# Kernel optimization log

Hardware: AMD Instinct MI355X
Metric: run time of the kernel (lower is better)

## Reference

```python
import jax, jax.numpy as jnp
import numpy as np

N, M, D = 131072, 8, 128
TAU = 1.0
E_CONST = float(np.e)


def setup_inputs() -> dict:
    key = jax.random.key(0)
    ks = jax.random.split(key, 6)
    x = jax.random.normal(ks[0], (N, M, D), dtype=jnp.float32)
    q = jax.random.uniform(ks[1], (N, M), dtype=jnp.float32)  # per-mode energies
    w = 0.1 * jax.random.uniform(ks[2], (M,), dtype=jnp.float32)
    b = 0.1 * jax.random.uniform(ks[3], (M,), dtype=jnp.float32)
    gammas = jax.random.uniform(ks[4], (M, M), dtype=jnp.float32)  # in (0,1)
    G = 0.1 * jax.random.normal(ks[5], (M,), dtype=jnp.float32)
    bias = jnp.zeros((M,), dtype=jnp.float32)
    qmin = jnp.zeros((M,), dtype=jnp.float32)
    return {"x": x, "q": q, "w": w, "b": b, "gammas": gammas,
            "G": G, "bias": bias, "qmin": qmin}


def reference(x, q, w, b, gammas, G, bias, qmin):
    e = jnp.float32(E_CONST)
    # correction (eval mode): shift by running min, clamp at e so phi > 0
    corr = jnp.maximum(q - qmin[None, :] + e, e)          # [N, M]
    phi = (1.0 + w)[None, :] * corr + b[None, :]          # [N, M]
    # symmetrized gamma: g[i,j] = gammas[min(i,j), max(i,j)]
    idx = jnp.arange(gammas.shape[0])
    g_sym = jnp.where(idx[:, None] < idx[None, :], gammas, gammas.T)  # [M, M]
    # pairwise power-weighted partial energies: phi_i^g * phi_j^(1-g)
    partials = phi[:, :, None] ** g_sym[None] * phi[:, None, :] ** (1.0 - g_sym)[None]  # [N, M, M]
    modal = jnp.sum(partials, axis=-1)                    # [N, M]
    logs = jax.nn.log_softmax(-TAU * modal, axis=-1)
    alphas = jnp.exp(logs)                                # [N, M]
    # gated attention over modes
    betas = jax.nn.relu(jnp.tanh(G[None, :] * alphas + bias[None, :]))  # [N, M]
    return betas[:, :, None] * x                          # [N, M, D]
```

## Files before the change

kernel.cpp:

```cpp
#include <hip/hip_runtime.h>
#include <math.h>

#define NROWS 131072
#define M 8
#define D 128
#define ROWS_PER_BLOCK 128
#define E_CONST 2.71828182845904523536f

__global__ __launch_bounds__(256) void emma_fused_kernel(
    const float* __restrict__ x, const float* __restrict__ q,
    const float* __restrict__ w, const float* __restrict__ b,
    const float* __restrict__ gammas, const float* __restrict__ G,
    const float* __restrict__ bias, const float* __restrict__ qmin,
    float* __restrict__ out)
{
    __shared__ float s_beta[ROWS_PER_BLOCK][M];
    __shared__ float s_g[M][M];
    __shared__ float s_w[M], s_b[M], s_G[M], s_bias[M], s_qmin[M];

    const int tid = threadIdx.x;

    if (tid < M * M) {
        int i = tid >> 3, j = tid & 7;
        s_g[i][j] = (i < j) ? gammas[i * M + j] : gammas[j * M + i];
    }
    if (tid >= 64 && tid < 64 + M) {
        int m = tid - 64;
        s_w[m]    = w[m];
        s_b[m]    = b[m];
        s_G[m]    = G[m];
        s_bias[m] = bias[m];
        s_qmin[m] = qmin[m];
    }
    __syncthreads();

    const int row0 = blockIdx.x * ROWS_PER_BLOCK;

    if (tid < ROWS_PER_BLOCK) {
        const int n = row0 + tid;
        const float4 q0 = *reinterpret_cast<const float4*>(q + (size_t)n * M);
        const float4 q1 = *reinterpret_cast<const float4*>(q + (size_t)n * M + 4);
        float qv[M] = {q0.x, q0.y, q0.z, q0.w, q1.x, q1.y, q1.z, q1.w};

        float lphi[M];
        #pragma unroll
        for (int m = 0; m < M; ++m) {
            float corr = fmaxf(qv[m] - s_qmin[m] + E_CONST, E_CONST);
            float phi  = (1.0f + s_w[m]) * corr + s_b[m];
            lphi[m] = logf(phi);
        }

        float modal[M];
        #pragma unroll
        for (int i = 0; i < M; ++i) {
            float s = 0.0f;
            #pragma unroll
            for (int j = 0; j < M; ++j) {
                float g = s_g[i][j];
                s += expf(fmaf(g, lphi[i] - lphi[j], lphi[j]));
            }
            modal[i] = s;
        }

        float mx = -modal[0];
        #pragma unroll
        for (int i = 1; i < M; ++i) mx = fmaxf(mx, -modal[i]);
        float esum = 0.0f;
        float ea[M];
        #pragma unroll
        for (int i = 0; i < M; ++i) {
            ea[i] = expf(-modal[i] - mx);
            esum += ea[i];
        }
        float inv = 1.0f / esum;

        #pragma unroll
        for (int m = 0; m < M; ++m) {
            float alpha = ea[m] * inv;
            float t = tanhf(fmaf(s_G[m], alpha, s_bias[m]));
            s_beta[tid][m] = fmaxf(t, 0.0f);
        }
    }
    __syncthreads();

    const size_t base = (size_t)row0 * (M * D);
    const float4* __restrict__ x4 = reinterpret_cast<const float4*>(x + base);
    float4* __restrict__ o4       = reinterpret_cast<float4*>(out + base);
    const int mm = tid >> 5;

    #pragma unroll 4
    for (int r = 0; r < ROWS_PER_BLOCK; ++r) {
        const float beta = s_beta[r][mm];
        float4 v = x4[(size_t)r * 256 + tid];
        v.x *= beta; v.y *= beta; v.z *= beta; v.w *= beta;
        o4[(size_t)r * 256 + tid] = v;
    }
}

extern "C" void kernel_launch(void* const* d_in, const int* in_sizes, int n_in,
                              void* d_out, int out_size, void* d_ws, size_t ws_size,
                              hipStream_t stream) {
    const float* x      = (const float*)d_in[0];
    const float* q      = (const float*)d_in[1];
    const float* w      = (const float*)d_in[2];
    const float* b      = (const float*)d_in[3];
    const float* gammas = (const float*)d_in[4];
    const float* G      = (const float*)d_in[5];
    const float* bias   = (const float*)d_in[6];
    const float* qmin   = (const float*)d_in[7];
    float* out = (float*)d_out;

    const int grid = NROWS / ROWS_PER_BLOCK;
    emma_fused_kernel<<<grid, 256, 0, stream>>>(x, q, w, b, gammas, G, bias, qmin, out);
}
```

Measured before the change: 217.8 us.

## Split fused kernel into beta-computation and grid-stride scaling kernels

```diff
diff --git a/kernel.cpp b/kernel.cpp
--- a/kernel.cpp
+++ b/kernel.cpp
@@ -4,9 +4,88 @@
 #define NROWS 131072
 #define M 8
 #define D 128
-#define ROWS_PER_BLOCK 128
 #define E_CONST 2.71828182845904523536f
 
+__global__ __launch_bounds__(256) void emma_beta_kernel(
+    const float* __restrict__ q,
+    const float* __restrict__ w, const float* __restrict__ b,
+    const float* __restrict__ gammas, const float* __restrict__ G,
+    const float* __restrict__ bias, const float* __restrict__ qmin,
+    float* __restrict__ betas)
+{
+    const int n = blockIdx.x * 256 + threadIdx.x;
+    if (n >= NROWS) return;
+
+    const float4 q0 = *reinterpret_cast<const float4*>(q + (size_t)n * M);
+    const float4 q1 = *reinterpret_cast<const float4*>(q + (size_t)n * M + 4);
+    float qv[M] = {q0.x, q0.y, q0.z, q0.w, q1.x, q1.y, q1.z, q1.w};
+
+    float lphi[M];
+    #pragma unroll
+    for (int m = 0; m < M; ++m) {
+        float corr = fmaxf(qv[m] - qmin[m] + E_CONST, E_CONST);
+        float phi  = (1.0f + w[m]) * corr + b[m];
+        lphi[m] = logf(phi);
+    }
+
+    float modal[M];
+    #pragma unroll
+    for (int i = 0; i < M; ++i) {
+        float s = 0.0f;
+        #pragma unroll
+        for (int j = 0; j < M; ++j) {
+            float g = (i < j) ? gammas[i * M + j] : gammas[j * M + i];
+            s += expf(fmaf(g, lphi[i] - lphi[j], lphi[j]));
+        }
+        modal[i] = s;
+    }
+
+    float mx = -modal[0];
+    #pragma unroll
+    for (int i = 1; i < M; ++i) mx = fmaxf(mx, -modal[i]);
+    float esum = 0.0f;
+    float ea[M];
+    #pragma unroll
+    for (int i = 0; i < M; ++i) {
+        ea[i] = expf(-modal[i] - mx);
+        esum += ea[i];
+    }
+    float inv = 1.0f / esum;
+
+    float4 o0, o1;
+    float bo[M];
+    #pragma unroll
+    for (int m = 0; m < M; ++m) {
+        float alpha = ea[m] * inv;
+        float t = tanhf(fmaf(G[m], alpha, bias[m]));
+        bo[m] = fmaxf(t, 0.0f);
+    }
+    o0.x = bo[0]; o0.y = bo[1]; o0.z = bo[2]; o0.w = bo[3];
+    o1.x = bo[4]; o1.y = bo[5]; o1.z = bo[6]; o1.w = bo[7];
+    *reinterpret_cast<float4*>(betas + (size_t)n * M)     = o0;
+    *reinterpret_cast<float4*>(betas + (size_t)n * M + 4) = o1;
+}
+
+#define NV4 ((size_t)NROWS * M * D / 4)
+#define SB_BLOCKS 2048
+
+__global__ __launch_bounds__(256) void emma_scale_kernel(
+    const float4* __restrict__ x4,
+    const float* __restrict__ betas,
+    float4* __restrict__ o4)
+{
+    size_t i = (size_t)blockIdx.x * 256 + threadIdx.x;
+    const size_t stride = (size_t)SB_BLOCKS * 256;
+    #pragma unroll 4
+    for (int k = 0; k < (int)(NV4 / stride); ++k, i += stride) {
+        const float bta = betas[i >> 5];
+        float4 v = x4[i];
+        v.x *= bta; v.y *= bta; v.z *= bta; v.w *= bta;
+        o4[i] = v;
+    }
+}
+
+#define ROWS_PER_BLOCK 128
 __global__ __launch_bounds__(256) void emma_fused_kernel(
     const float* __restrict__ x, const float* __restrict__ q,
     const float* __restrict__ w, const float* __restrict__ b,
@@ -15,25 +94,7 @@
     float* __restrict__ out)
 {
     __shared__ float s_beta[ROWS_PER_BLOCK][M];
-    __shared__ float s_g[M][M];
-    __shared__ float s_w[M], s_b[M], s_G[M], s_bias[M], s_qmin[M];
-
     const int tid = threadIdx.x;
-
-    if (tid < M * M) {
-        int i = tid >> 3, j = tid & 7;
-        s_g[i][j] = (i < j) ? gammas[i * M + j] : gammas[j * M + i];
-    }
-    if (tid >= 64 && tid < 64 + M) {
-        int m = tid - 64;
-        s_w[m]    = w[m];
-        s_b[m]    = b[m];
-        s_G[m]    = G[m];
-        s_bias[m] = bias[m];
-        s_qmin[m] = qmin[m];
-    }
-    __syncthreads();
-
     const int row0 = blockIdx.x * ROWS_PER_BLOCK;
 
     if (tid < ROWS_PER_BLOCK) {
@@ -41,43 +102,35 @@
         const float4 q0 = *reinterpret_cast<const float4*>(q + (size_t)n * M);
         const float4 q1 = *reinterpret_cast<const float4*>(q + (size_t)n * M + 4);
         float qv[M] = {q0.x, q0.y, q0.z, q0.w, q1.x, q1.y, q1.z, q1.w};
-
         float lphi[M];
         #pragma unroll
         for (int m = 0; m < M; ++m) {
-            float corr = fmaxf(qv[m] - s_qmin[m] + E_CONST, E_CONST);
-            float phi  = (1.0f + s_w[m]) * corr + s_b[m];
+            float corr = fmaxf(qv[m] - qmin[m] + E_CONST, E_CONST);
+            float phi  = (1.0f + w[m]) * corr + b[m];
             lphi[m] = logf(phi);
         }
-
         float modal[M];
         #pragma unroll
         for (int i = 0; i < M; ++i) {
             float s = 0.0f;
             #pragma unroll
             for (int j = 0; j < M; ++j) {
-                float g = s_g[i][j];
+                float g = (i < j) ? gammas[i * M + j] : gammas[j * M + i];
                 s += expf(fmaf(g, lphi[i] - lphi[j], lphi[j]));
             }
             modal[i] = s;
         }
-
         float mx = -modal[0];
         #pragma unroll
         for (int i = 1; i < M; ++i) mx = fmaxf(mx, -modal[i]);
         float esum = 0.0f;
         float ea[M];
         #pragma unroll
-        for (int i = 0; i < M; ++i) {
-            ea[i] = expf(-modal[i] - mx);
-            esum += ea[i];
-        }
+        for (int i = 0; i < M; ++i) { ea[i] = expf(-modal[i] - mx); esum += ea[i]; }
         float inv = 1.0f / esum;
-
         #pragma unroll
         for (int m = 0; m < M; ++m) {
-            float alpha = ea[m] * inv;
-            float t = tanhf(fmaf(s_G[m], alpha, s_bias[m]));
+            float t = tanhf(fmaf(G[m], ea[m] * inv, bias[m]));
             s_beta[tid][m] = fmaxf(t, 0.0f);
         }
     }
@@ -87,7 +140,6 @@
     const float4* __restrict__ x4 = reinterpret_cast<const float4*>(x + base);
     float4* __restrict__ o4       = reinterpret_cast<float4*>(out + base);
     const int mm = tid >> 5;
-
     #pragma unroll 4
     for (int r = 0; r < ROWS_PER_BLOCK; ++r) {
         const float beta = s_beta[r][mm];
@@ -110,6 +162,15 @@
     const float* qmin   = (const float*)d_in[7];
     float* out = (float*)d_out;
 
-    const int grid = NROWS / ROWS_PER_BLOCK;
-    emma_fused_kernel<<<grid, 256, 0, stream>>>(x, q, w, b, gammas, G, bias, qmin, out);
+    const size_t beta_bytes = (size_t)NROWS * M * sizeof(float);
+    if (ws_size >= beta_bytes) {
+        float* betas = (float*)d_ws;
+        emma_beta_kernel<<<NROWS / 256, 256, 0, stream>>>(
+            q, w, b, gammas, G, bias, qmin, betas);
+        emma_scale_kernel<<<SB_BLOCKS, 256, 0, stream>>>(
+            (const float4*)x, betas, (float4*)out);
+    } else {
+        emma_fused_kernel<<<NROWS / ROWS_PER_BLOCK, 256, 0, stream>>>(
+            x, q, w, b, gammas, G, bias, qmin, out);
+    }
 }
```

After: 261.0 us. 19.8% more time.

## Spread modal softmax across 8 lanes per row with shuffle reductions

Applied to the files above, without the earlier changes.

```diff
diff --git a/kernel.cpp b/kernel.cpp
--- a/kernel.cpp
+++ b/kernel.cpp
@@ -4,40 +4,24 @@
 #define NROWS 131072
 #define M 8
 #define D 128
-#define ROWS_PER_BLOCK 128
+#define RPB 32
 #define E_CONST 2.71828182845904523536f
 
-__global__ __launch_bounds__(256) void emma_fused_kernel(
+__global__ __launch_bounds__(256) void emma_fused2(
     const float* __restrict__ x, const float* __restrict__ q,
     const float* __restrict__ w, const float* __restrict__ b,
     const float* __restrict__ gammas, const float* __restrict__ G,
     const float* __restrict__ bias, const float* __restrict__ qmin,
     float* __restrict__ out)
 {
-    __shared__ float s_beta[ROWS_PER_BLOCK][M];
-    __shared__ float s_g[M][M];
-    __shared__ float s_w[M], s_b[M], s_G[M], s_bias[M], s_qmin[M];
+    __shared__ float s_beta[RPB][M];
 
     const int tid = threadIdx.x;
+    const int r   = tid >> 3;
+    const int i   = tid & 7;
+    const int n   = blockIdx.x * RPB + r;
 
-    if (tid < M * M) {
-        int i = tid >> 3, j = tid & 7;
-        s_g[i][j] = (i < j) ? gammas[i * M + j] : gammas[j * M + i];
-    }
-    if (tid >= 64 && tid < 64 + M) {
-        int m = tid - 64;
-        s_w[m]    = w[m];
-        s_b[m]    = b[m];
-        s_G[m]    = G[m];
-        s_bias[m] = bias[m];
-        s_qmin[m] = qmin[m];
-    }
-    __syncthreads();
-
-    const int row0 = blockIdx.x * ROWS_PER_BLOCK;
-
-    if (tid < ROWS_PER_BLOCK) {
-        const int n = row0 + tid;
+    {
         const float4 q0 = *reinterpret_cast<const float4*>(q + (size_t)n * M);
         const float4 q1 = *reinterpret_cast<const float4*>(q + (size_t)n * M + 4);
         float qv[M] = {q0.x, q0.y, q0.z, q0.w, q1.x, q1.y, q1.z, q1.w};
@@ -45,55 +29,50 @@
         float lphi[M];
         #pragma unroll
         for (int m = 0; m < M; ++m) {
-            float corr = fmaxf(qv[m] - s_qmin[m] + E_CONST, E_CONST);
-            float phi  = (1.0f + s_w[m]) * corr + s_b[m];
+            float corr = fmaxf(qv[m] - qmin[m] + E_CONST, E_CONST);
+            float phi  = fmaf(w[m], corr, corr) + b[m];
             lphi[m] = logf(phi);
         }
 
-        float modal[M];
+        float myl = lphi[0];
         #pragma unroll
-        for (int i = 0; i < M; ++i) {
-            float s = 0.0f;
-            #pragma unroll
-            for (int j = 0; j < M; ++j) {
-                float g = s_g[i][j];
-                s += expf(fmaf(g, lphi[i] - lphi[j], lphi[j]));
-            }
-            modal[i] = s;
+        for (int m = 1; m < M; ++m) if (i == m) myl = lphi[m];
+
+        float s = 0.0f;
+        #pragma unroll
+        for (int j = 0; j < M; ++j) {
+            int lo = (i < j) ? i : j;
+            int hi = (i < j) ? j : i;
+            float g = gammas[lo * M + hi];
+            s += expf(fmaf(g, myl - lphi[j], lphi[j]));
         }
 
-        float mx = -modal[0];
+        float neg = -s;
+        float mx = neg;
         #pragma unroll
-        for (int i = 1; i < M; ++i) mx = fmaxf(mx, -modal[i]);
-        float esum = 0.0f;
-        float ea[M];
+        for (int d = 1; d < 8; d <<= 1) mx = fmaxf(mx, __shfl_xor(mx, d, 8));
+        float e = expf(neg - mx);
+        float sum = e;
         #pragma unroll
-        for (int i = 0; i < M; ++i) {
-            ea[i] = expf(-modal[i] - mx);
-            esum += ea[i];
-        }
-        float inv = 1.0f / esum;
+        for (int d = 1; d < 8; d <<= 1) sum += __shfl_xor(sum, d, 8);
+        float alpha = e / sum;
 
-        #pragma unroll
-        for (int m = 0; m < M; ++m) {
-            float alpha = ea[m] * inv;
-            float t = tanhf(fmaf(s_G[m], alpha, s_bias[m]));
-            s_beta[tid][m] = fmaxf(t, 0.0f);
-        }
+        float t = tanhf(fmaf(G[i], alpha, bias[i]));
+        s_beta[r][i] = fmaxf(t, 0.0f);
     }
     __syncthreads();
 
-    const size_t base = (size_t)row0 * (M * D);
+    const size_t base = (size_t)blockIdx.x * (RPB * M * D);
     const float4* __restrict__ x4 = reinterpret_cast<const float4*>(x + base);
     float4* __restrict__ o4       = reinterpret_cast<float4*>(out + base);
     const int mm = tid >> 5;
 
     #pragma unroll 4
-    for (int r = 0; r < ROWS_PER_BLOCK; ++r) {
-        const float beta = s_beta[r][mm];
-        float4 v = x4[(size_t)r * 256 + tid];
+    for (int rr = 0; rr < RPB; ++rr) {
+        const float beta = s_beta[rr][mm];
+        float4 v = x4[(size_t)rr * 256 + tid];
         v.x *= beta; v.y *= beta; v.z *= beta; v.w *= beta;
-        o4[(size_t)r * 256 + tid] = v;
+        o4[(size_t)rr * 256 + tid] = v;
     }
 }
 
@@ -110,6 +89,6 @@
     const float* qmin   = (const float*)d_in[7];
     float* out = (float*)d_out;
 
-    const int grid = NROWS / ROWS_PER_BLOCK;
-    emma_fused_kernel<<<grid, 256, 0, stream>>>(x, q, w, b, gammas, G, bias, qmin, out);
+    emma_fused2<<<NROWS / RPB, 256, 0, stream>>>(
+        x, q, w, b, gammas, G, bias, qmin, out);
 }
```

Measured after the change: 214.6 us. About the same (-1.5%).
